# Optimization experiments

Measured on AMD Instinct MI355X. Metric: run time of the kernel, lower is better.

The kernel has to match this reference:

```python
import jax, jax.numpy as jnp
import numpy as np

DISPS = (8, 8, 4, 2)
STRIDES = (2, 1, 1, 1)
DG = 4      # deformable groups
PAD = 1     # (kernel_size-1)//2 for k=3
KH = KW = 3


def pointwise_corr(f1, f2, disp, stride):
    """Windowed pointwise cross-correlation.
    f1, f2: [B, C, H, W]. Returns [B, (2d+1)^2, H, W], dy-major shift order,
    displacement step = stride, normalized by channel count.
    """
    B, C, H, W = f1.shape
    pad = disp * stride
    f2p = jnp.pad(f2, ((0, 0), (0, 0), (pad, pad), (pad, pad)))
    rng = np.arange(2 * disp + 1) * stride
    shifts = np.stack(np.meshgrid(rng, rng, indexing='ij'), -1).reshape(-1, 2)
    shifts = jnp.asarray(shifts, jnp.int32)

    def one(s):
        f2s = jax.lax.dynamic_slice(f2p, (0, 0, s[0], s[1]), (B, C, H, W))
        return jnp.sum(f1 * f2s, axis=1) / C   # [B, H, W]

    corr = jax.vmap(one)(shifts)               # [K2, B, H, W]
    return jnp.transpose(corr, (1, 0, 2, 3))


def bilinear_sample(img, y, x):
    """img: [cg, H, W]; y, x: [K2, H, W] float sample coords.
    Zero outside boundaries (deform-conv semantics). Returns [cg, K2, H, W]."""
    cg, H, W = img.shape
    y0 = jnp.floor(y); x0 = jnp.floor(x)
    wy = y - y0;       wx = x - x0
    y0i = y0.astype(jnp.int32); x0i = x0.astype(jnp.int32)

    def gather(iy, ix):
        valid = (iy >= 0) & (iy < H) & (ix >= 0) & (ix < W)
        v = img[:, jnp.clip(iy, 0, H - 1), jnp.clip(ix, 0, W - 1)]  # [cg,K2,H,W]
        return v * valid.astype(img.dtype)

    v00 = gather(y0i,     x0i)
    v01 = gather(y0i,     x0i + 1)
    v10 = gather(y0i + 1, x0i)
    v11 = gather(y0i + 1, x0i + 1)
    return (v00 * (1 - wy) * (1 - wx) + v01 * (1 - wy) * wx
            + v10 * wy * (1 - wx) + v11 * wy * wx)


def deform_conv(x, offset, weight, dg, pad):
    """Deformable conv v1, stride 1. x: [N,C,H,W]; offset: [N, dg*2*K2, H, W]
    (per group, per kernel point, (dy,dx)); weight: [O, C, kh, kw]."""
    N, C, H, W = x.shape
    O, _, kh, kw = weight.shape
    K2 = kh * kw
    cg = C // dg
    off = offset.reshape(N, dg, K2, 2, H, W)
    ky, kx = np.meshgrid(np.arange(kh), np.arange(kw), indexing='ij')
    ky = jnp.asarray(ky.reshape(-1), jnp.float32)
    kx = jnp.asarray(kx.reshape(-1), jnp.float32)
    gy = jnp.arange(H, dtype=jnp.float32)
    gx = jnp.arange(W, dtype=jnp.float32)
    base_y = ky[:, None, None] - pad + gy[None, :, None]   # [K2,H,1]
    base_x = kx[:, None, None] - pad + gx[None, None, :]   # [K2,1,W]
    ys = base_y[None, None] + off[:, :, :, 0]              # [N,dg,K2,H,W]
    xs = base_x[None, None] + off[:, :, :, 1]
    xg = x.reshape(N, dg, cg, H, W)
    sampled = jax.vmap(jax.vmap(bilinear_sample))(xg, ys, xs)  # [N,dg,cg,K2,H,W]
    w = weight.reshape(O, dg, cg, K2)
    return jnp.einsum('ogck,ngckhw->nohw', w, sampled)


def _forward_single(x, w_off, w_adapt, disp, stride):
    T, B, C, H, W = x.shape
    corrs = [pointwise_corr(x[t], x[t - 1], disp, stride) for t in range(1, T)]
    corr = jnp.concatenate(corrs, axis=0)                   # [(T-1)*B, K2, H, W]
    offset = jnp.einsum('ok,bkhw->bohw', w_off, corr)       # 1x1 conv, no bias
    feat_in = x[1:].reshape((T - 1) * B, C, H, W)
    feat = jax.nn.relu(deform_conv(feat_in, offset, w_adapt, DG, PAD))
    return jnp.concatenate([x[0], feat], axis=0)            # [T*B, C, H, W]


def setup_inputs() -> dict:
    key = jax.random.key(0)
    ks = jax.random.split(key, 12)
    shapes = [(2, 2, 256, 64, 64), (2, 2, 256, 32, 32),
              (2, 2, 256, 16, 16), (2, 2, 256, 8, 8)]
    d = {}
    for i, s in enumerate(shapes):
        d[f"x{i}"] = jax.random.normal(ks[i], s, jnp.float32)
    for i, disp in enumerate(DISPS):
        K2 = (2 * disp + 1) ** 2
        d[f"w_off{i}"] = 0.01 * jax.random.normal(ks[4 + i], (DG * 2 * KH * KW, K2), jnp.float32)
        d[f"w_adapt{i}"] = 0.01 * jax.random.normal(ks[8 + i], (256, 256, KH, KW), jnp.float32)
    return d


def reference(x0, x1, x2, x3, w_off0, w_off1, w_off2, w_off3,
              w_adapt0, w_adapt1, w_adapt2, w_adapt3):
    xs = [x0, x1, x2, x3]
    w_offs = [w_off0, w_off1, w_off2, w_off3]
    w_adapts = [w_adapt0, w_adapt1, w_adapt2, w_adapt3]
    outs = [_forward_single(xs[l], w_offs[l], w_adapts[l], DISPS[l], STRIDES[l])
            for l in range(4)]
    return tuple(outs)
```

## Files before the change

kernel.cpp:

```cpp
#include <hip/hip_runtime.h>

typedef unsigned int u32;
typedef unsigned short u16;
typedef _Float16 f16x2 __attribute__((ext_vector_type(2)));
typedef _Float16 f16x8 __attribute__((ext_vector_type(8)));
typedef __bf16 bf16x8 __attribute__((ext_vector_type(8)));
typedef float f32x4 __attribute__((ext_vector_type(4)));

static __device__ __forceinline__ f16x2 bch(u32 u) { return __builtin_bit_cast(f16x2, u); }


__global__ __launch_bounds__(256) void prep_kernel(
    const float* __restrict__ x0, const float* __restrict__ x1,
    const float* __restrict__ x2, const float* __restrict__ x3,
    const float* __restrict__ w0, const float* __restrict__ w1,
    const float* __restrict__ w2, const float* __restrict__ w3,
    u32* __restrict__ xq, u16* __restrict__ A, float* __restrict__ offs,
    float* __restrict__ out)
{
  __shared__ u32 plds[32 * 65];
  int bx = blockIdx.x, t = threadIdx.x;
  if (bx < 3060) {
    int i = bx * 256 + t;
    if (i < 783360) offs[i] = 0.f;
    return;
  }
  if (bx < 4420) {
    int local = bx - 3060;
    const float* xs; int lvlb, lgW, lgnch;
    if (local < 1024)      { xs = x0; lvlb = 0;       lgW = 6; lgnch = 6; }
    else if (local < 1280) { xs = x1; lvlb = 2097152; lgW = 5; lgnch = 4; local -= 1024; }
    else if (local < 1344) { xs = x2; lvlb = 2621440; lgW = 4; lgnch = 2; local -= 1280; }
    else                   { xs = x3; lvlb = 2752512; lgW = 3; lgnch = 0; local -= 1344; }
    int HW = 1 << (2 * lgW);
    int hc = local & ((1 << lgnch) - 1);
    int g  = (local >> lgnch) & 3;
    int tb = local >> (lgnch + 2);
    int hw0 = hc * 64;
    int lane = t & 63, qd = t >> 6;
#pragma unroll
    for (int j = 0; j < 8; ++j) {
      int cpw = qd * 8 + j;
      int c = tb * 256 + g * 64 + cpw * 2;
      const float* s = xs + (size_t)c * HW + hw0 + lane;
      float f0 = s[0], f1 = s[HW];
      f16x2 h; h[0] = (_Float16)f0; h[1] = (_Float16)f1;
      plds[cpw * 65 + lane] = __builtin_bit_cast(u32, h);
    }
    __syncthreads();
    u32* dst = xq + lvlb + (size_t)(tb * 4 + g) * HW * 32 + (size_t)hw0 * 32;
#pragma unroll
    for (int j = 0; j < 8; ++j) {
      int ow = j * 256 + t;
      int hwl = ow >> 5, ww = ow & 31;
      dst[(size_t)hwl * 32 + ww] = plds[ww * 65 + hwl];
    }
    return;
  }
  if (bx < 13636) {
    int i = (bx - 4420) * 256 + t;
    if (i >= 2359296) return;
    int lv = i / 589824;
    const float* w = (lv == 0) ? w0 : (lv == 1) ? w1 : (lv == 2) ? w2 : w3;
    int local = i - lv * 589824;
    int o = local / 2304;
    int k = local - o * 2304;
    int g = k / 576;
    int r = k - g * 576;
    int p = r >> 6;
    int c = r & 63;
    float v = w[(size_t)(o * 256 + g * 64 + c) * 9 + p];
    __bf16 bv = (__bf16)v;
    A[i] = __builtin_bit_cast(u16, bv);
    return;
  }
  {
    int i = (bx - 13636) * 256 + t;
    const float* xs; int base, dstb;
    if (i < 2097152)      { xs = x0; base = 0;       dstb = 0; }
    else if (i < 2621440) { xs = x1; base = 2097152; dstb = 4194304; }
    else if (i < 2752512) { xs = x2; base = 2621440; dstb = 5242880; }
    else if (i < 2785280) { xs = x3; base = 2752512; dstb = 5505024; }
    else return;
    int local = i - base;
    out[(size_t)dstb + local] = xs[local];
  }
}

__global__ __launch_bounds__(256) void corr_mfma_kernel(const u32* __restrict__ xq, float* __restrict__ corr)
{
  __shared__ __align__(16) u32 lds[8192];
  int t = threadIdx.x, bx = blockIdx.x;

  if (bx >= 1472) {
    int gw = ((bx - 1472) * 256 + t) >> 6;
    int lane = t & 63;
    int cs = lane >> 4, hwi = lane & 15;
    int obase = gw * 16;
    int K2, R, DISP, lgW, xqlb, crb, rel;
    if (obase < 41472)      { K2 = 81; R = 9; DISP = 4; lgW = 4; xqlb = 2621440; crb = 2959360; rel = obase; }
    else if (obase < 44672) { K2 = 25; R = 5; DISP = 2; lgW = 3; xqlb = 2752512; crb = 3000832; rel = obase - 41472; }
    else return;
    int W = 1 << lgW, HW = W * W;
    int hw = (rel & (HW - 1)) + hwi;
    int rr = rel >> (2 * lgW);
    int k = rr % K2, b = rr / K2;
    int h = hw >> lgW, wc = hw & (W - 1);
    int dy = k / R - DISP, dx = k % R - DISP;
    int h2 = h + dy, w2 = wc + dx;
    float a = 0.f;
    if ((u32)h2 < (u32)W && (u32)w2 < (u32)W) {
      const u32* q1 = xq + xqlb + ((size_t)((2 + b) * 4 + cs) * HW + hw) * 32;
      const u32* q0 = xq + xqlb + ((size_t)(b * 4 + cs) * HW + (h2 * W + w2)) * 32;
#pragma unroll 8
      for (int j = 0; j < 32; ++j)
        a = __builtin_amdgcn_fdot2(bch(q1[j]), bch(q0[j]), a, false);
    }
    a += __shfl_xor(a, 16);
    a += __shfl_xor(a, 32);
    if (cs == 0) corr[crb + rel + hwi] = a * 0.00390625f;
    return;
  }

  int l = t & 63, w = t >> 6;
  int lvl, b, y, kq, lgW, W, HW, xqlb, crb;
  if (bx < 1152) { lvl = 0; int r = bx;        kq = r % 9; r /= 9; y = r & 63; b = r >> 6;
                   lgW = 6; W = 64; HW = 4096; xqlb = 0;       crb = 0; }
  else           { lvl = 1; int r = bx - 1152; kq = r % 5; r /= 5; y = r & 31; b = r >> 5;
                   lgW = 5; W = 32; HW = 1024; xqlb = 2097152; crb = 2367488; }
  int par, qy, storeok;
  if (lvl == 0) { int rr = w >> 1; par = w & 1; qy = (kq < 8) ? 2 * kq + rr : 16;
                  storeok = !(kq == 8 && w >= 2); }
  else          { par = 0; qy = 4 * kq + w; storeok = (qy <= 16); if (qy > 16) qy = 16; }
  int rowY = (lvl == 0) ? (y + 2 * qy - 16) : (y + qy - 8);
  int f1words = (lvl == 0) ? 1024 : 512;
  int tb1 = 2 + b, tb0 = b;

  bool f1do = (lvl == 0) || (w < 2);
  u32 f1_lo; int f1_dw;
  {
    int G = w * 64 + l;
    int px = G >> 2, s = G & 3;
    int i = px & 31;
    int pari = px >> 5;
    int x = (lvl == 0) ? (2 * i + pari) : px;
    int cg = (s ^ ((i & 3) ^ ((i >> 2) & 3))) & 3;
    f1_lo = (u32)(xqlb + (y * W + x) * 32 + cg * 4);
    f1_dw = w * 256;
  }
  u32 f2_lo[3], f2_mask[3]; int f2_dw[3];
#pragma unroll
  for (int q = 0; q < 3; ++q) {
    int F = q * 64 + l;
    int jp = F >> 2, s = F & 3;
    int cg = (s ^ ((jp & 3) ^ ((jp >> 2) & 3))) & 3;
    int xs = (lvl == 0) ? (2 * (jp - 8) + par) : (jp - 8);
    bool valid = ((u32)xs < (u32)W) && ((u32)rowY < (u32)W);
    f2_lo[q]   = valid ? (u32)(xqlb + (rowY * W + xs) * 32 + cg * 4) : 6968960u;
    f2_mask[q] = valid ? 0xFFFFFFFFu : 0u;
    f2_dw[q]   = f1words + w * 768 + q * 256;
  }
  int lr = l & 15, lk = l >> 4;
  int aoff[2], boff[3];
#pragma unroll
  for (int it = 0; it < 2; ++it) {
    int iA = it * 16 + lr;
    int px = ((lvl == 0) ? par * 32 : 0) + iA;
    int phys = (lk ^ ((iA & 3) ^ ((iA >> 2) & 3))) & 3;
    aoff[it] = (px * 16 + phys * 4) * 4;
  }
#pragma unroll
  for (int T = 0; T < 3; ++T) {
    int jp = T * 16 + lr;
    int phys = (lk ^ ((jp & 3) ^ ((jp >> 2) & 3))) & 3;
    boff[T] = (f1words + w * 768 + jp * 16 + phys * 4) * 4;
  }

  f32x4 acc0 = {0,0,0,0}, acc1 = {0,0,0,0}, acc2 = {0,0,0,0}, acc3 = {0,0,0,0};

  auto issue = [&](int ch, int sel) {
    int g2 = ch >> 1, hf = ch & 1;
    u32 cb1 = ((u32)(tb1 * 4 + g2) * (u32)HW) * 32u + (u32)hf * 16u;
    u32 cb0 = ((u32)(tb0 * 4 + g2) * (u32)HW) * 32u + (u32)hf * 16u;
    u32* lb = &lds[sel * 4096];
    if (f1do)
      __builtin_amdgcn_global_load_lds(xq + cb1 + f1_lo, lb + f1_dw, 16, 0, 0);
#pragma unroll
    for (int q = 0; q < 3; ++q)
      __builtin_amdgcn_global_load_lds(xq + ((cb0 & f2_mask[q]) + f2_lo[q]), lb + f2_dw[q], 16, 0, 0);
  };

  issue(0, 0);
#pragma unroll 1
  for (int ch = 0; ch < 8; ++ch) {
    int sel = ch & 1;
    asm volatile("s_waitcnt vmcnt(0)" ::: "memory");
    asm volatile("s_barrier" ::: "memory");
    __builtin_amdgcn_sched_barrier(0);
    if (ch < 7) issue(ch + 1, sel ^ 1);
    const char* lb = (const char*)&lds[sel * 4096];
    f16x8 A0 = *(const f16x8*)(lb + aoff[0]);
    f16x8 A1 = *(const f16x8*)(lb + aoff[1]);
    f16x8 B0 = *(const f16x8*)(lb + boff[0]);
    f16x8 B1 = *(const f16x8*)(lb + boff[1]);
    f16x8 B2 = *(const f16x8*)(lb + boff[2]);
    acc0 = __builtin_amdgcn_mfma_f32_16x16x32_f16(A0, B0, acc0, 0, 0, 0);
    acc1 = __builtin_amdgcn_mfma_f32_16x16x32_f16(A0, B1, acc1, 0, 0, 0);
    acc2 = __builtin_amdgcn_mfma_f32_16x16x32_f16(A1, B1, acc2, 0, 0, 0);
    acc3 = __builtin_amdgcn_mfma_f32_16x16x32_f16(A1, B2, acc3, 0, 0, 0);
  }

  if (!storeok) return;
  const float sc = 0.00390625f;
#pragma unroll
  for (int tile = 0; tile < 4; ++tile) {
    int it = (tile >= 2) ? 1 : 0;
    int T  = (tile == 0) ? 0 : (tile == 3) ? 2 : 1;
    f32x4 av = (tile == 0) ? acc0 : (tile == 1) ? acc1 : (tile == 2) ? acc2 : acc3;
    int jp = T * 16 + lr;
#pragma unroll
    for (int jj = 0; jj < 4; ++jj) {
      int i = it * 16 + lk * 4 + jj;
      int qx = jp - i;
      if (qx >= 0 && qx <= 16) {
        int xo = (lvl == 0) ? (2 * i + par) : i;
        int k = qy * 17 + qx;
        corr[crb + (size_t)(b * 289 + k) * HW + y * W + xo] = av[jj] * sc;
      }
    }
  }
}

__global__ __launch_bounds__(256) void offset_kernel(
    const float* __restrict__ corr,
    const float* __restrict__ wo0, const float* __restrict__ wo1,
    const float* __restrict__ wo2, const float* __restrict__ wo3,
    float* __restrict__ offs)
{
  int t = threadIdx.x, bx = blockIdx.x;
  int kc = bx % 6;
  int unit = bx / 6;
  int og = unit & 3;
  int pb = unit >> 2;

  int lgW, K2, crb, ofb, pbl;
  const float* wo;
  if (pb < 32)      { pbl = pb;      lgW = 6; K2 = 289; crb = 0;       ofb = 0;      wo = wo0; }
  else if (pb < 40) { pbl = pb - 32; lgW = 5; K2 = 289; crb = 2367488; ofb = 589824; wo = wo1; }
  else if (pb < 42) { pbl = pb - 40; lgW = 4; K2 = 81;  crb = 2959360; ofb = 737280; wo = wo2; }
  else              { pbl = 0;       lgW = 3; K2 = 25;  crb = 3000832; ofb = 774144; wo = wo3; }
  int HW = 1 << (2 * lgW);
  int pxg = pbl * 256 + t;
  if (lgW == 3 && t >= 128) return;
  int b = pxg >> (2 * lgW);
  int hw = pxg & (HW - 1);

  int kchunk = (K2 + 5) / 6;
  int klo = kc * kchunk;
  int khi = klo + kchunk; if (khi > K2) khi = K2;
  if (klo >= khi) return;

  const float* cr = corr + crb + (size_t)b * K2 * HW + hw;
  const float* wp = wo + (size_t)og * 18 * K2;
  float acc[18];
#pragma unroll
  for (int j = 0; j < 18; ++j) acc[j] = 0.f;
#pragma unroll 2
  for (int k = klo; k < khi; ++k) {
    float cv = cr[(size_t)k * HW];
#pragma unroll
    for (int j = 0; j < 18; ++j) acc[j] = fmaf(wp[(size_t)j * K2 + k], cv, acc[j]);
  }
  float* op = offs + ofb + ((size_t)b * 72 + og * 18) * HW + hw;
#pragma unroll
  for (int j = 0; j < 18; ++j) atomicAdd(&op[(size_t)j * HW], acc[j]);
}

__global__ __launch_bounds__(256) void sample_kernel(
    const u32* __restrict__ xq, const float* __restrict__ offs,
    u16* __restrict__ Bbuf, int Rg0, int nrows)
{
  int tid = blockIdx.x * 256 + threadIdx.x;
  if (tid >= nrows * 144) return;
  int r_l = tid / 144;
  int rem = tid - r_l * 144;
  int gp = rem >> 2, cq = rem & 3;
  int Rg = Rg0 + r_l;
  int b, hw, lgW, xqlb, ofb;
  if (Rg < 8192)       { b = Rg >> 12;       hw = Rg & 4095;  lgW = 6; xqlb = 0;       ofb = 0; }
  else if (Rg < 10240) { int r = Rg - 8192;  b = r >> 10; hw = r & 1023; lgW = 5; xqlb = 2097152; ofb = 589824; }
  else if (Rg < 10752) { int r = Rg - 10240; b = r >> 8;  hw = r & 255;  lgW = 4; xqlb = 2621440; ofb = 737280; }
  else                 { int r = Rg - 10752; b = r >> 6;  hw = r & 63;   lgW = 3; xqlb = 2752512; ofb = 774144; }
  int W = 1 << lgW, HW = W * W;
  u16* rowp = Bbuf + (size_t)r_l * 2304;

  size_t ob = (size_t)ofb + ((size_t)b * 72 + gp * 2) * HW + hw;
  float ody = offs[ob], odx = offs[ob + HW];
  int g = gp / 9, p = gp - g * 9;
  int ky = p / 3, kx = p - ky * 3;
  int sh = hw >> lgW, sw = hw & (W - 1);
  float ys = (float)(sh + ky - 1) + ody;
  float xs = (float)(sw + kx - 1) + odx;
  float y0f = floorf(ys), x0f = floorf(xs);
  float wy = ys - y0f, wx = xs - x0f;
  int y0 = (int)y0f, x0 = (int)x0f, y1 = y0 + 1, x1 = x0 + 1;
  bool vy0 = (u32)y0 < (u32)W, vy1 = (u32)y1 < (u32)W;
  bool vx0 = (u32)x0 < (u32)W, vx1 = (u32)x1 < (u32)W;
  float w00 = (1.f - wy) * (1.f - wx), w01 = (1.f - wy) * wx;
  float w10 = wy * (1.f - wx), w11 = wy * wx;
  const u32* base = xq + xqlb + ((size_t)((2 + b) * 4 + g) * HW) * 32 + cq * 8;
  const uint4 z = make_uint4(0, 0, 0, 0);
  uint4 a00 = z, c00 = z, a01 = z, c01 = z, a10 = z, c10 = z, a11 = z, c11 = z;
  if (vy0 && vx0) { const u32* p0 = base + (size_t)(y0 * W + x0) * 32; a00 = *(const uint4*)p0; c00 = *(const uint4*)(p0 + 4); }
  if (vy0 && vx1) { const u32* p0 = base + (size_t)(y0 * W + x1) * 32; a01 = *(const uint4*)p0; c01 = *(const uint4*)(p0 + 4); }
  if (vy1 && vx0) { const u32* p0 = base + (size_t)(y1 * W + x0) * 32; a10 = *(const uint4*)p0; c10 = *(const uint4*)(p0 + 4); }
  if (vy1 && vx1) { const u32* p0 = base + (size_t)(y1 * W + x1) * 32; a11 = *(const uint4*)p0; c11 = *(const uint4*)(p0 + 4); }
  bf16x8 r0, r1;
#pragma unroll
  for (int ww = 0; ww < 4; ++ww) {
    f16x2 h00 = bch(((const u32*)&a00)[ww]);
    f16x2 h01 = bch(((const u32*)&a01)[ww]);
    f16x2 h10 = bch(((const u32*)&a10)[ww]);
    f16x2 h11 = bch(((const u32*)&a11)[ww]);
    float lo = w00 * (float)h00[0] + w01 * (float)h01[0] + w10 * (float)h10[0] + w11 * (float)h11[0];
    float hi = w00 * (float)h00[1] + w01 * (float)h01[1] + w10 * (float)h10[1] + w11 * (float)h11[1];
    r0[2 * ww] = (__bf16)lo; r0[2 * ww + 1] = (__bf16)hi;
  }
#pragma unroll
  for (int ww = 0; ww < 4; ++ww) {
    f16x2 h00 = bch(((const u32*)&c00)[ww]);
    f16x2 h01 = bch(((const u32*)&c01)[ww]);
    f16x2 h10 = bch(((const u32*)&c10)[ww]);
    f16x2 h11 = bch(((const u32*)&c11)[ww]);
    float lo = w00 * (float)h00[0] + w01 * (float)h01[0] + w10 * (float)h10[0] + w11 * (float)h11[0];
    float hi = w00 * (float)h00[1] + w01 * (float)h01[1] + w10 * (float)h10[1] + w11 * (float)h11[1];
    r1[2 * ww] = (__bf16)lo; r1[2 * ww + 1] = (__bf16)hi;
  }
  u16* dst = rowp + gp * 64 + cq * 16;
  *(bf16x8*)dst = r0;
  *(bf16x8*)(dst + 8) = r1;
}

__global__ __launch_bounds__(256) void gemm2_kernel(
    const u16* __restrict__ A, const u16* __restrict__ Bbuf,
    int Rg0, float* __restrict__ out)
{
  __shared__ __align__(16) u16 Al[64 * 72];
  __shared__ __align__(16) u16 Bl[32 * 72];
  int t = threadIdx.x, bx = blockIdx.x;
  int mt = bx & 3, nt = bx >> 2;
  int Rgt = Rg0 + nt * 32;
  int b, hw0, lgW, Ab, outb;
  if (Rgt < 8192)       { b = Rgt >> 12;       hw0 = Rgt & 4095;  lgW = 6; Ab = 0;       outb = 2097152; }
  else if (Rgt < 10240) { int r = Rgt - 8192;  b = r >> 10; hw0 = r & 1023; lgW = 5; Ab = 589824;  outb = 4718592; }
  else if (Rgt < 10752) { int r = Rgt - 10240; b = r >> 8;  hw0 = r & 255;  lgW = 4; Ab = 1179648; outb = 5373952; }
  else                  { int r = Rgt - 10752; b = r >> 6;  hw0 = r & 63;   lgW = 3; Ab = 1769472; outb = 5537792; }
  int HW = 1 << (2 * lgW);
  const u16* Bbase = Bbuf + (size_t)(Rgt - Rg0) * 2304;

  int o0 = mt * 64;
  int l = t & 63, wv = t >> 6;
  int lr = l & 15, lk = l >> 4;
  int wvr = wv >> 1, wvc = wv & 1;

  int arow = t >> 2, ac4 = t & 3;
  int brow = t >> 3, bc8 = t & 7;
  const u16* Asrc = A + Ab + (size_t)(o0 + arow) * 2304 + ac4 * 16;
  const u16* Bsrc = Bbase + (size_t)brow * 2304 + bc8 * 8;

  f32x4 acc0 = {0, 0, 0, 0}, acc1 = {0, 0, 0, 0};
  uint4 ar0, ar1, br;
  auto issue = [&](int k0) {
    const uint4* as = (const uint4*)(Asrc + k0);
    ar0 = as[0]; ar1 = as[1];
    br = *(const uint4*)(Bsrc + k0);
  };
  auto commit = [&]() {
    *(uint4*)(&Al[arow * 72 + ac4 * 16]) = ar0;
    *(uint4*)(&Al[arow * 72 + ac4 * 16 + 8]) = ar1;
    *(uint4*)(&Bl[brow * 72 + bc8 * 8]) = br;
  };
  issue(0); commit();
  __syncthreads();
#pragma unroll 1
  for (int kt = 0; kt < 36; ++kt) {
    if (kt < 35) issue((kt + 1) * 64);
#pragma unroll
    for (int kk = 0; kk < 2; ++kk) {
      bf16x8 b0 = *(const bf16x8*)(&Bl[(wvc * 16 + lr) * 72 + kk * 32 + lk * 8]);
      bf16x8 a0 = *(const bf16x8*)(&Al[(wvr * 32 + lr) * 72 + kk * 32 + lk * 8]);
      bf16x8 a1 = *(const bf16x8*)(&Al[(wvr * 32 + 16 + lr) * 72 + kk * 32 + lk * 8]);
      acc0 = __builtin_amdgcn_mfma_f32_16x16x32_bf16(a0, b0, acc0, 0, 0, 0);
      acc1 = __builtin_amdgcn_mfma_f32_16x16x32_bf16(a1, b0, acc1, 0, 0, 0);
    }
    __syncthreads();
    if (kt < 35) { commit(); __syncthreads(); }
  }
  float* op = out + outb + (size_t)b * 256 * HW;
#pragma unroll
  for (int j = 0; j < 4; ++j) {
    int orow = o0 + wvr * 32 + lk * 4 + j;
    int col = hw0 + wvc * 16 + lr;
    op[(size_t)orow * HW + col]        = fmaxf(acc0[j], 0.f);
    op[(size_t)(orow + 16) * HW + col] = fmaxf(acc1[j], 0.f);
  }
}

extern "C" void kernel_launch(void* const* d_in, const int* in_sizes, int n_in,
                              void* d_out, int out_size, void* d_ws, size_t ws_size,
                              hipStream_t stream) {
  const float* x[4];
  const float* woff[4];
  const float* wad[4];
  for (int l = 0; l < 4; ++l) {
    x[l]    = (const float*)d_in[l];
    woff[l] = (const float*)d_in[4 + 2 * l];
    wad[l]  = (const float*)d_in[5 + 2 * l];
  }
  float* out = (float*)d_out;
  char* ws = (char*)d_ws;
  u32*   xq   = (u32*)(ws);
  u16*   A    = (u16*)(ws + 11141120);
  float* corr = (float*)(ws + 15859712);
  float* offs = (float*)(ws + 27875840);
  u16* BbufS = (u16*)(ws + 15859712);
  u16* BbufL = (u16*)(ws + 31009280);
  int big = (ws_size >= (size_t)81144320) ? 1 : 0;

  prep_kernel<<<24516, 256, 0, stream>>>(x[0], x[1], x[2], x[3],
                                         wad[0], wad[1], wad[2], wad[3], xq, A, offs, out);
  corr_mfma_kernel<<<2170, 256, 0, stream>>>(xq, corr);
  offset_kernel<<<1032, 256, 0, stream>>>(corr, woff[0], woff[1], woff[2], woff[3], offs);

  if (big) {
    sample_kernel<<<6120, 256, 0, stream>>>(xq, offs, BbufL, 0, 10880);
    gemm2_kernel<<<1360, 256, 0, stream>>>(A, BbufL, 0, out);
  } else {
    for (int ph = 0; ph < 5; ++ph) {
      int Rg0 = ph * 2560;
      int nrows = (ph < 4) ? 2560 : 640;
      int sgrid = (nrows * 144 + 255) / 256;
      int ggrid = (nrows / 32) * 4;
      sample_kernel<<<sgrid, 256, 0, stream>>>(xq, offs, BbufS, Rg0, nrows);
      gemm2_kernel<<<ggrid, 256, 0, stream>>>(A, BbufS, Rg0, out);
    }
  }
}
```

Before: 138.4 us.

## Widen gemm2 N-tile to 64 and double-buffer LDS with one barrier per step

The deform-conv GEMM block tile grows from 64x32 to 64x64, so each wave now runs four MFMAs per k-substep and A-tile reuse doubles. LDS becomes double-buffered: the next tile is committed to the alternate buffer and the one after is prefetched, leaving one __syncthreads per k-step instead of two. The aim is less global traffic for A and fewer barrier stalls. The cost is half as many blocks (680), which lowers parallelism across CUs, plus more LDS and registers per block.

```diff
diff --git a/kernel.cpp b/kernel.cpp
--- a/kernel.cpp
+++ b/kernel.cpp
@@ -345,11 +345,11 @@
     const u16* __restrict__ A, const u16* __restrict__ Bbuf,
     int Rg0, float* __restrict__ out)
 {
-  __shared__ __align__(16) u16 Al[64 * 72];
-  __shared__ __align__(16) u16 Bl[32 * 72];
+  __shared__ __align__(16) u16 Al[2][64 * 72];
+  __shared__ __align__(16) u16 Bl[2][64 * 72];
   int t = threadIdx.x, bx = blockIdx.x;
   int mt = bx & 3, nt = bx >> 2;
-  int Rgt = Rg0 + nt * 32;
+  int Rgt = Rg0 + nt * 64;
   int b, hw0, lgW, Ab, outb;
   if (Rgt < 8192)       { b = Rgt >> 12;       hw0 = Rgt & 4095;  lgW = 6; Ab = 0;       outb = 2097152; }
   else if (Rgt < 10240) { int r = Rgt - 8192;  b = r >> 10; hw0 = r & 1023; lgW = 5; Ab = 589824;  outb = 4718592; }
@@ -363,47 +363,63 @@
   int lr = l & 15, lk = l >> 4;
   int wvr = wv >> 1, wvc = wv & 1;
 
-  int arow = t >> 2, ac4 = t & 3;
-  int brow = t >> 3, bc8 = t & 7;
-  const u16* Asrc = A + Ab + (size_t)(o0 + arow) * 2304 + ac4 * 16;
-  const u16* Bsrc = Bbase + (size_t)brow * 2304 + bc8 * 8;
-
-  f32x4 acc0 = {0, 0, 0, 0}, acc1 = {0, 0, 0, 0};
-  uint4 ar0, ar1, br;
-  auto issue = [&](int k0) {
-    const uint4* as = (const uint4*)(Asrc + k0);
-    ar0 = as[0]; ar1 = as[1];
-    br = *(const uint4*)(Bsrc + k0);
+  int srow = t >> 2, sc4 = t & 3;
+  const u16* Asrc = A + Ab + (size_t)(o0 + srow) * 2304 + sc4 * 16;
+  const u16* Bsrc = Bbase + (size_t)srow * 2304 + sc4 * 16;
+
+  f32x4 acc[2][2];
+#pragma unroll
+  for (int i = 0; i < 2; ++i)
+#pragma unroll
+    for (int j = 0; j < 2; ++j) acc[i][j] = (f32x4){0, 0, 0, 0};
+
+  uint4 pa0, pa1, pb0, pb1;
+  auto issue = [&](int kt) {
+    const uint4* as = (const uint4*)(Asrc + kt * 64);
+    const uint4* bs = (const uint4*)(Bsrc + kt * 64);
+    pa0 = as[0]; pa1 = as[1];
+    pb0 = bs[0]; pb1 = bs[1];
   };
-  auto commit = [&]() {
-    *(uint4*)(&Al[arow * 72 + ac4 * 16]) = ar0;
-    *(uint4*)(&Al[arow * 72 + ac4 * 16 + 8]) = ar1;
-    *(uint4*)(&Bl[brow * 72 + bc8 * 8]) = br;
+  auto commit = [&](int sel) {
+    *(uint4*)(&Al[sel][srow * 72 + sc4 * 16]) = pa0;
+    *(uint4*)(&Al[sel][srow * 72 + sc4 * 16 + 8]) = pa1;
+    *(uint4*)(&Bl[sel][srow * 72 + sc4 * 16]) = pb0;
+    *(uint4*)(&Bl[sel][srow * 72 + sc4 * 16 + 8]) = pb1;
   };
-  issue(0); commit();
+
+  issue(0); commit(0);
+  issue(1);
   __syncthreads();
 #pragma unroll 1
   for (int kt = 0; kt < 36; ++kt) {
-    if (kt < 35) issue((kt + 1) * 64);
+    int sel = kt & 1;
 #pragma unroll
     for (int kk = 0; kk < 2; ++kk) {
-      bf16x8 b0 = *(const bf16x8*)(&Bl[(wvc * 16 + lr) * 72 + kk * 32 + lk * 8]);
-      bf16x8 a0 = *(const bf16x8*)(&Al[(wvr * 32 + lr) * 72 + kk * 32 + lk * 8]);
-      bf16x8 a1 = *(const bf16x8*)(&Al[(wvr * 32 + 16 + lr) * 72 + kk * 32 + lk * 8]);
-      acc0 = __builtin_amdgcn_mfma_f32_16x16x32_bf16(a0, b0, acc0, 0, 0, 0);
-      acc1 = __builtin_amdgcn_mfma_f32_16x16x32_bf16(a1, b0, acc1, 0, 0, 0);
-    }
+      bf16x8 b0 = *(const bf16x8*)(&Bl[sel][(wvc * 32 + lr) * 72 + kk * 32 + lk * 8]);
+      bf16x8 b1 = *(const bf16x8*)(&Bl[sel][(wvc * 32 + 16 + lr) * 72 + kk * 32 + lk * 8]);
+      bf16x8 a0 = *(const bf16x8*)(&Al[sel][(wvr * 32 + lr) * 72 + kk * 32 + lk * 8]);
+      bf16x8 a1 = *(const bf16x8*)(&Al[sel][(wvr * 32 + 16 + lr) * 72 + kk * 32 + lk * 8]);
+      acc[0][0] = __builtin_amdgcn_mfma_f32_16x16x32_bf16(a0, b0, acc[0][0], 0, 0, 0);
+      acc[0][1] = __builtin_amdgcn_mfma_f32_16x16x32_bf16(a0, b1, acc[0][1], 0, 0, 0);
+      acc[1][0] = __builtin_amdgcn_mfma_f32_16x16x32_bf16(a1, b0, acc[1][0], 0, 0, 0);
+      acc[1][1] = __builtin_amdgcn_mfma_f32_16x16x32_bf16(a1, b1, acc[1][1], 0, 0, 0);
+    }
+    if (kt < 35) commit(sel ^ 1);
+    if (kt < 34) issue(kt + 2);
     __syncthreads();
-    if (kt < 35) { commit(); __syncthreads(); }
-  }
+  }
+
   float* op = out + outb + (size_t)b * 256 * HW;
 #pragma unroll
-  for (int j = 0; j < 4; ++j) {
-    int orow = o0 + wvr * 32 + lk * 4 + j;
-    int col = hw0 + wvc * 16 + lr;
-    op[(size_t)orow * HW + col]        = fmaxf(acc0[j], 0.f);
-    op[(size_t)(orow + 16) * HW + col] = fmaxf(acc1[j], 0.f);
-  }
+  for (int ar = 0; ar < 2; ++ar)
+#pragma unroll
+    for (int bc = 0; bc < 2; ++bc)
+#pragma unroll
+      for (int j = 0; j < 4; ++j) {
+        int orow = o0 + wvr * 32 + ar * 16 + lk * 4 + j;
+        int col = hw0 + wvc * 32 + bc * 16 + lr;
+        op[(size_t)orow * HW + col] = fmaxf(acc[ar][bc][j], 0.f);
+      }
 }
 
 extern "C" void kernel_launch(void* const* d_in, const int* in_sizes, int n_in,
@@ -434,13 +450,13 @@
 
   if (big) {
     sample_kernel<<<6120, 256, 0, stream>>>(xq, offs, BbufL, 0, 10880);
-    gemm2_kernel<<<1360, 256, 0, stream>>>(A, BbufL, 0, out);
+    gemm2_kernel<<<680, 256, 0, stream>>>(A, BbufL, 0, out);
   } else {
     for (int ph = 0; ph < 5; ++ph) {
       int Rg0 = ph * 2560;
       int nrows = (ph < 4) ? 2560 : 640;
       int sgrid = (nrows * 144 + 255) / 256;
-      int ggrid = (nrows / 32) * 4;
+      int ggrid = (nrows / 64) * 4;
       sample_kernel<<<sgrid, 256, 0, stream>>>(xq, offs, BbufS, Rg0, nrows);
       gemm2_kernel<<<ggrid, 256, 0, stream>>>(A, BbufS, Rg0, out);
     }
```

Result: faster. 132.9 us (-4.0%).
